# Kernel optimization log

Hardware: AMD Instinct MI355X
Metric: run time of the kernel (lower is better)

Reference implementation:

```python
import jax, jax.numpy as jnp
import numpy as np

ROPE_DIM = 64
NOPE_DIM = 128
KV_LORA_RANK = 512
B, H, S = 4, 16, 1024


def setup_inputs() -> dict:
    key = jax.random.key(0)
    k1, k2, k3 = jax.random.split(key, 3)
    q_nope_with_k_up = jax.random.normal(k1, (B, H, S, KV_LORA_RANK), dtype=jnp.float32)
    compressed_kv = jax.random.normal(k2, (B, S, KV_LORA_RANK), dtype=jnp.float32)
    rope_attention = jax.random.normal(k3, (B, H, S, S), dtype=jnp.float32)
    mask = jnp.zeros((B, S), dtype=jnp.int32)  # key padding mask; 1 = masked
    return {
        "q_nope_with_k_up": q_nope_with_k_up,
        "compressed_kv": compressed_kv,
        "rope_attention": rope_attention,
        "mask": mask,
        "have_causal_mask": 1,
    }


def reference(q_nope_with_k_up, compressed_kv, rope_attention, mask, have_causal_mask):
    # nope scores: [B,H,S,S] = q [B,H,S,r] @ kv^T [B,1,r,S]
    nope = jnp.einsum("bhqr,bkr->bhqk", q_nope_with_k_up, compressed_kv)
    scale = 1.0 / np.float32(np.sqrt(ROPE_DIM + NOPE_DIM))
    scores = (rope_attention + nope) * scale
    if mask is not None:
        m = mask[:, None, None, :]  # [B,1,1,S]
        if have_causal_mask:
            s = scores.shape[-1]
            causal = jnp.triu(jnp.ones((s, s), dtype=jnp.int32), 1)[None, None]  # [1,1,S,S]
            m = jnp.where(causal == 1, causal, m)  # combined mask, 1 = masked
        scores = jnp.where(m == 1, -jnp.inf, scores)
    attn = jax.nn.softmax(scores, axis=-1)
    # AV with shared compressed latent: [B,H,S,S] @ [B,1,S,r] -> [B,H,S,r]
    return jnp.einsum("bhqk,bkr->bhqr", attn, compressed_kv)
```

## Files before the change

### kernel.cpp

```cpp
#include <hip/hip_runtime.h>
#include <math.h>

#define B_ 4
#define H_ 16
#define S_ 1024
#define R_ 512
#define BQ 64
#define BK 32
#define NTHREADS 512
#define NKS 16

typedef unsigned short u16;
typedef unsigned int   u32;
typedef short bf16x8 __attribute__((ext_vector_type(8)));
typedef float f32x4  __attribute__((ext_vector_type(4)));

__device__ inline u16 f2bf(float x) {
    union { float f; u32 u; } v; v.f = x;
    return (u16)((v.u + 0x7fffu + ((v.u >> 16) & 1u)) >> 16);
}
__device__ inline u32 pack2(float a, float b) {
    return (u32)f2bf(a) | ((u32)f2bf(b) << 16);
}

#define MFMA16(a, b, c) __builtin_amdgcn_mfma_f32_16x16x32_bf16(a, b, c, 0, 0, 0)

__device__ inline void gload16(const void* g, void* l) {
    __builtin_amdgcn_global_load_lds(
        (const __attribute__((address_space(1))) void*)g,
        (__attribute__((address_space(3))) void*)l,
        16, 0, 0);
}

#define RAW_BARRIER() do {                                 \
    asm volatile("s_waitcnt lgkmcnt(0)" ::: "memory");     \
    __builtin_amdgcn_s_barrier();                          \
    asm volatile("" ::: "memory");                         \
} while (0)

__global__ __launch_bounds__(256)
void mla_prep_kernel(const float* __restrict__ ckv,
                     u16* __restrict__ ckv_bf,
                     u16* __restrict__ ckvT)
{
    const int tid = threadIdx.x;
    const int k0 = blockIdx.x * 64;
    const int r0 = blockIdx.y * 64;
    const int b  = blockIdx.z;

    __shared__ u16 sT[64][72];

    const float* src = ckv + ((size_t)b * S_ + k0) * R_ + r0;
    u16* obf = ckv_bf + ((size_t)b * S_ + k0) * R_ + r0;

    #pragma unroll
    for (int i = 0; i < 2; ++i) {
        int idx = tid + i * 256;
        int kk  = idx >> 3;
        int c8  = idx & 7;
        int csrc = c8 ^ (kk & 7);
        const float* p = src + (size_t)kk * R_ + csrc * 8;
        float4 f0 = *(const float4*)p;
        float4 f1 = *(const float4*)(p + 4);
        u32 w0 = pack2(f0.x, f0.y), w1 = pack2(f0.z, f0.w);
        u32 w2 = pack2(f1.x, f1.y), w3 = pack2(f1.z, f1.w);
        u32* dst = (u32*)(obf + (size_t)kk * R_ + c8 * 8);
        dst[0] = w0; dst[1] = w1; dst[2] = w2; dst[3] = w3;
        u16 e[8] = {(u16)w0,(u16)(w0>>16),(u16)w1,(u16)(w1>>16),
                    (u16)w2,(u16)(w2>>16),(u16)w3,(u16)(w3>>16)};
        #pragma unroll
        for (int j = 0; j < 8; ++j) sT[csrc * 8 + j][kk] = e[j];
    }
    __syncthreads();

    u16* obT = ckvT + (size_t)b * R_ * S_;
    #pragma unroll
    for (int i = 0; i < 2; ++i) {
        int idx = tid + i * 256;
        int rr = idx >> 3;
        int kc = idx & 7;
        const u16* s = &sT[rr][kc * 8];
        u32* dd = (u32*)(obT + (size_t)(r0 + rr) * S_ + k0 + kc * 8);
        dd[0] = (u32)s[0] | ((u32)s[1] << 16);
        dd[1] = (u32)s[2] | ((u32)s[3] << 16);
        dd[2] = (u32)s[4] | ((u32)s[5] << 16);
        dd[3] = (u32)s[6] | ((u32)s[7] << 16);
    }
}

__global__ __attribute__((amdgpu_waves_per_eu(2, 2)))
__launch_bounds__(NTHREADS)
void mla_attn_kernel(const float* __restrict__ qn,
                     const float* __restrict__ rope,
                     const int*   __restrict__ mask,
                     const int*   __restrict__ cmaskp,
                     const u16*   __restrict__ ckv_bf,
                     const u16*   __restrict__ ckvT,
                     float*       __restrict__ out)
{
    const int tid  = threadIdx.x;
    const int lane = tid & 63;
    const int wv   = tid >> 6;
    const int l15  = lane & 15;
    const int lq   = lane >> 4;
    const int qg   = wv >> 1;
    const int ktg  = wv & 1;

    const int qt = (int)gridDim.x - 1 - (int)blockIdx.x;
    const int h  = blockIdx.y;
    const int b  = blockIdx.z;
    const int q0 = qt * BQ;

    const int cflag = cmaskp[0];

    __shared__ __align__(16) u16 sCKV [2][BK][R_];
    __shared__ __align__(16) u16 sCKVT[2][R_][BK];
    __shared__ __align__(16) u16 sP[BQ][40];

    bf16x8 aq[NKS];
    {
        const float* qrow = qn + ((size_t)((b * H_ + h) * S_ + q0 + qg * 16 + l15)) * R_;
        #pragma unroll
        for (int s = 0; s < NKS; ++s) {
            const float* p = qrow + 32 * s + lq * 8;
            float4 f0 = *(const float4*)p;
            float4 f1 = *(const float4*)(p + 4);
            union { u32 u[4]; bf16x8 v; } cv;
            cv.u[0] = pack2(f0.x, f0.y); cv.u[1] = pack2(f0.z, f0.w);
            cv.u[2] = pack2(f1.x, f1.y); cv.u[3] = pack2(f1.z, f1.w);
            aq[s] = cv.v;
        }
    }

    f32x4 acc[4][4];
    #pragma unroll
    for (int i = 0; i < 4; ++i)
        #pragma unroll
        for (int j = 0; j < 4; ++j)
            acc[i][j] = (f32x4){0.f, 0.f, 0.f, 0.f};

    float m_run[4], l_run[4];
    #pragma unroll
    for (int r = 0; r < 4; ++r) { m_run[r] = -INFINITY; l_run[r] = 0.0f; }

    const u16*   ckvb  = ckv_bf + (size_t)b * S_ * R_;
    const u16*   ckvTb = ckvT   + (size_t)b * R_ * S_;
    const float* ropeb = rope + ((size_t)(b * H_ + h)) * S_ * S_;
    const int*   maskb = mask + b * S_;

    const int nkt = cflag ? ((q0 + BQ) / BK) : (S_ / BK);
    const float SCALE = 0.07216878364870323f;
    const int rowg0 = q0 + qg * 16 + 4 * lq;

    float rp[4];
    int   mkv;

    {
        char* lA = (char*)&sCKV [0][0][0] + wv * 1024;
        char* lT = (char*)&sCKVT[0][0][0] + wv * 1024;
        #pragma unroll
        for (int rd = 0; rd < 4; ++rd) {
            u32 o = (u32)(rd * 8192 + tid * 16);
            gload16((const char*)ckvb + o, lA + rd * 8192);
            gload16((const char*)ckvTb + (size_t)(o >> 6) * 2048 + (o & 63),
                    lT + rd * 8192);
        }
        #pragma unroll
        for (int reg = 0; reg < 4; ++reg)
            rp[reg] = ropeb[(size_t)(rowg0 + reg) * S_ + ktg * 16 + l15];
        mkv = maskb[ktg * 16 + l15];
    }
    __syncthreads();

    for (int kt = 0; kt < nkt; ++kt) {
        const int d  = kt & 1;
        const int k0 = kt * BK;
        const bool more = (kt + 1 < nkt);
        float rp_n[4];
        int   mkv_n = 0;

        if (more) {
            const int k0n = k0 + BK;
            const char* gA = (const char*)ckvb  + (size_t)k0n * 1024;
            const char* gT = (const char*)ckvTb + (size_t)k0n * 2;
            char* lA = (char*)&sCKV [d ^ 1][0][0] + wv * 1024;
            char* lT = (char*)&sCKVT[d ^ 1][0][0] + wv * 1024;
            #pragma unroll
            for (int rd = 0; rd < 4; ++rd) {
                u32 o = (u32)(rd * 8192 + tid * 16);
                gload16(gA + o, lA + rd * 8192);
                gload16(gT + (size_t)(o >> 6) * 2048 + (o & 63), lT + rd * 8192);
            }
            #pragma unroll
            for (int reg = 0; reg < 4; ++reg)
                rp_n[reg] = ropeb[(size_t)(rowg0 + reg) * S_ + k0n + ktg * 16 + l15];
            mkv_n = maskb[k0n + ktg * 16 + l15];
        }

        f32x4 sc0 = {0.f,0.f,0.f,0.f}, sc1 = {0.f,0.f,0.f,0.f};
        {
            const char* base = (const char*)&sCKV[d][0][0];
            const u32 rowb = (u32)(ktg * 16 + l15) * 1024;
            const u32 swz  = ((u32)(l15 & 7)) << 4;
            #pragma unroll
            for (int s = 0; s < NKS; s += 2) {
                bf16x8 bf0 = *(const bf16x8*)(base + rowb +
                                (((u32)(64 * s)      + (u32)(16 * lq)) ^ swz));
                bf16x8 bf1 = *(const bf16x8*)(base + rowb +
                                (((u32)(64 * s + 64) + (u32)(16 * lq)) ^ swz));
                sc0 = MFMA16(aq[s],     bf0, sc0);
                sc1 = MFMA16(aq[s + 1], bf1, sc1);
            }
        }

        float scf[4], vm[4];
        {
            const int colg = k0 + ktg * 16 + l15;
            #pragma unroll
            for (int reg = 0; reg < 4; ++reg) {
                float v = (sc0[reg] + sc1[reg] + rp[reg]) * SCALE;
                if (mkv) v = -INFINITY;
                if (cflag && colg > rowg0 + reg) v = -INFINITY;
                scf[reg] = v;
                vm[reg]  = v;
            }
            #pragma unroll
            for (int m = 1; m <= 8; m <<= 1)
                #pragma unroll
                for (int reg = 0; reg < 4; ++reg)
                    vm[reg] = fmaxf(vm[reg], __shfl_xor(vm[reg], m));
            if (l15 == 0) {
                #pragma unroll
                for (int reg = 0; reg < 4; ++reg)
                    *(float*)&sP[qg * 16 + 4 * lq + reg][34 + 2 * ktg] = vm[reg];
            }
        }
        RAW_BARRIER();

        {
            float pv[4], alpha[4], rs[4];
            #pragma unroll
            for (int reg = 0; reg < 4; ++reg) {
                float pm = *(const float*)&sP[qg * 16 + 4 * lq + reg][34 + 2 * (ktg ^ 1)];
                float mn = fmaxf(m_run[reg], fmaxf(vm[reg], pm));
                if (mn == -INFINITY) {
                    alpha[reg] = 1.0f; pv[reg] = 0.0f;
                } else {
                    alpha[reg] = __expf(m_run[reg] - mn);
                    pv[reg]    = __expf(scf[reg] - mn);
                }
                m_run[reg] = mn;
                rs[reg] = pv[reg];
            }
            #pragma unroll
            for (int m = 1; m <= 8; m <<= 1)
                #pragma unroll
                for (int reg = 0; reg < 4; ++reg)
                    rs[reg] += __shfl_xor(rs[reg], m);
            #pragma unroll
            for (int reg = 0; reg < 4; ++reg) {
                l_run[reg] = l_run[reg] * alpha[reg] + rs[reg];
                sP[qg * 16 + 4 * lq + reg][ktg * 16 + l15] = f2bf(pv[reg]);
            }
            if (ktg == 0 && l15 == 0) {
                #pragma unroll
                for (int reg = 0; reg < 4; ++reg)
                    *(float*)&sP[qg * 16 + 4 * lq + reg][32] = alpha[reg];
            }
        }
        RAW_BARRIER();

        {
            float alr[4][4];
            #pragma unroll
            for (int mi = 0; mi < 4; ++mi)
                #pragma unroll
                for (int reg = 0; reg < 4; ++reg)
                    alr[mi][reg] = *(const float*)&sP[mi * 16 + 4 * lq + reg][32];
            #pragma unroll
            for (int mi = 0; mi < 4; ++mi)
                #pragma unroll
                for (int ni = 0; ni < 4; ++ni)
                    #pragma unroll
                    for (int reg = 0; reg < 4; ++reg)
                        acc[mi][ni][reg] *= alr[mi][reg];

            const int kq = lq * 8;
            bf16x8 af[4], bfr[4];
            #pragma unroll
            for (int mi = 0; mi < 4; ++mi)
                af[mi] = *(const bf16x8*)&sP[mi * 16 + l15][kq];
            const char* tbase = (const char*)&sCKVT[d][0][0];
            #pragma unroll
            for (int ni = 0; ni < 4; ++ni)
                bfr[ni] = *(const bf16x8*)(tbase +
                            (u32)(wv * 64 + ni * 16 + l15) * 64 + (u32)(lq * 16));
            #pragma unroll
            for (int mi = 0; mi < 4; ++mi)
                #pragma unroll
                for (int ni = 0; ni < 4; ++ni)
                    acc[mi][ni] = MFMA16(af[mi], bfr[ni], acc[mi][ni]);
        }
        __syncthreads();

        #pragma unroll
        for (int reg = 0; reg < 4; ++reg) rp[reg] = more ? rp_n[reg] : rp[reg];
        mkv = more ? mkv_n : mkv;
    }

    if (l15 == 0) {
        #pragma unroll
        for (int reg = 0; reg < 4; ++reg)
            *(float*)&sP[qg * 16 + 4 * lq + reg][34 + 2 * ktg] = l_run[reg];
    }
    __syncthreads();

    float linv[4][4];
    #pragma unroll
    for (int mi = 0; mi < 4; ++mi)
        #pragma unroll
        for (int reg = 0; reg < 4; ++reg) {
            int row = mi * 16 + 4 * lq + reg;
            float lt = *(const float*)&sP[row][34] + *(const float*)&sP[row][36];
            linv[mi][reg] = 1.0f / lt;
        }

    float* ob = out + ((size_t)((b * H_ + h) * S_ + q0)) * R_;
    #pragma unroll
    for (int mi = 0; mi < 4; ++mi)
        #pragma unroll
        for (int ni = 0; ni < 4; ++ni)
            #pragma unroll
            for (int reg = 0; reg < 4; ++reg)
                ob[(size_t)(mi * 16 + 4 * lq + reg) * R_ + wv * 64 + ni * 16 + l15]
                    = acc[mi][ni][reg] * linv[mi][reg];
}

extern "C" void kernel_launch(void* const* d_in, const int* in_sizes, int n_in,
                              void* d_out, int out_size, void* d_ws, size_t ws_size,
                              hipStream_t stream)
{
    (void)in_sizes; (void)n_in; (void)out_size; (void)ws_size;
    const float* qn   = (const float*)d_in[0];
    const float* ckv  = (const float*)d_in[1];
    const float* rope = (const float*)d_in[2];
    const int*   mask = (const int*)d_in[3];
    const int*   cm   = (const int*)d_in[4];
    float* out = (float*)d_out;

    u16* ckv_bf = (u16*)d_ws;
    u16* ckvT   = ckv_bf + (size_t)B_ * S_ * R_;

    hipLaunchKernelGGL(mla_prep_kernel, dim3(S_ / 64, R_ / 64, B_), dim3(256),
                       0, stream, ckv, ckv_bf, ckvT);
    hipLaunchKernelGGL(mla_attn_kernel, dim3(S_ / BQ, H_, B_), dim3(NTHREADS),
                       0, stream, qn, rope, mask, cm, ckv_bf, ckvT, out);
}
```

Baseline: 842.1 us.

## Software-pipeline QK and PV stages with BK=64, one barrier per iteration

Doubles the key tile to 64 and restructures the loop so the softmax/PV stage of tile kt-1 overlaps with the QK stage of tile kt, using double-buffered P and metadata buffers and a single __syncthreads per iteration instead of three barriers. The transposed latent is no longer staged through LDS; PV B-fragments are read directly from global memory. P writes use an XOR swizzle, and s_setprio brackets the MFMA regions. This cuts barrier count and LDS traffic but adds register pressure and puts direct global loads on the PV path, which may stall if they miss cache.

```diff
diff --git a/kernel.cpp b/kernel.cpp
--- a/kernel.cpp
+++ b/kernel.cpp
@@ -6,7 +6,7 @@
 #define S_ 1024
 #define R_ 512
 #define BQ 64
-#define BK 32
+#define BK 64
 #define NTHREADS 512
 #define NKS 16
 
@@ -31,12 +31,6 @@
         (__attribute__((address_space(3))) void*)l,
         16, 0, 0);
 }
-
-#define RAW_BARRIER() do {                                 \
-    asm volatile("s_waitcnt lgkmcnt(0)" ::: "memory");     \
-    __builtin_amdgcn_s_barrier();                          \
-    asm volatile("" ::: "memory");                         \
-} while (0)
 
 __global__ __launch_bounds__(256)
 void mla_prep_kernel(const float* __restrict__ ckv,
@@ -113,9 +107,10 @@
 
     const int cflag = cmaskp[0];
 
-    __shared__ __align__(16) u16 sCKV [2][BK][R_];
-    __shared__ __align__(16) u16 sCKVT[2][R_][BK];
-    __shared__ __align__(16) u16 sP[BQ][40];
+    __shared__ __align__(16) u16   sCKV[2][BK][R_];
+    __shared__ __align__(16) u16   sPP[2][BQ][BK];
+    __shared__ __align__(16) float sMeta[2][BQ][4];
+    __shared__ __align__(16) f32x4 sAlpha[2][16];
 
     bf16x8 aq[NKS];
     {
@@ -148,81 +143,101 @@
     const float* ropeb = rope + ((size_t)(b * H_ + h)) * S_ * S_;
     const int*   maskb = mask + b * S_;
 
-    const int nkt = cflag ? ((q0 + BQ) / BK) : (S_ / BK);
+    const int nkt = cflag ? (qt + 1) : (S_ / BK);
     const float SCALE = 0.07216878364870323f;
     const int rowg0 = q0 + qg * 16 + 4 * lq;
 
-    float rp[4];
-    int   mkv;
+    float rp[2][4], rpn[2][4];
+    int   mkv[2], mkvn[2];
+    float scp[2][4];
+    float vmp[4];
+    bf16x8 bfr[4][2];
 
     {
-        char* lA = (char*)&sCKV [0][0][0] + wv * 1024;
-        char* lT = (char*)&sCKVT[0][0][0] + wv * 1024;
-        #pragma unroll
-        for (int rd = 0; rd < 4; ++rd) {
-            u32 o = (u32)(rd * 8192 + tid * 16);
-            gload16((const char*)ckvb + o, lA + rd * 8192);
-            gload16((const char*)ckvTb + (size_t)(o >> 6) * 2048 + (o & 63),
-                    lT + rd * 8192);
-        }
-        #pragma unroll
-        for (int reg = 0; reg < 4; ++reg)
-            rp[reg] = ropeb[(size_t)(rowg0 + reg) * S_ + ktg * 16 + l15];
-        mkv = maskb[ktg * 16 + l15];
+        char* lA = (char*)&sCKV[0][0][0] + wv * 1024;
+        const char* gA = (const char*)ckvb;
+        #pragma unroll
+        for (int rd = 0; rd < 8; ++rd) {
+            u32 o = (u32)(rd * 8192 + wv * 1024 + (lane & 63) * 16);
+            gload16(gA + o, lA + rd * 8192);
+        }
+        const float* rb2 = ropeb + (size_t)rowg0 * S_ + ktg * 32 + l15;
+        #pragma unroll
+        for (int reg = 0; reg < 4; ++reg) {
+            rp[0][reg] = rb2[(size_t)reg * S_];
+            rp[1][reg] = rb2[(size_t)reg * S_ + 16];
+        }
+        mkv[0] = maskb[ktg * 32 + l15];
+        mkv[1] = maskb[ktg * 32 + 16 + l15];
     }
     __syncthreads();
 
-    for (int kt = 0; kt < nkt; ++kt) {
-        const int d  = kt & 1;
-        const int k0 = kt * BK;
-        const bool more = (kt + 1 < nkt);
-        float rp_n[4];
-        int   mkv_n = 0;
-
-        if (more) {
-            const int k0n = k0 + BK;
-            const char* gA = (const char*)ckvb  + (size_t)k0n * 1024;
-            const char* gT = (const char*)ckvTb + (size_t)k0n * 2;
-            char* lA = (char*)&sCKV [d ^ 1][0][0] + wv * 1024;
-            char* lT = (char*)&sCKVT[d ^ 1][0][0] + wv * 1024;
-            #pragma unroll
-            for (int rd = 0; rd < 4; ++rd) {
-                u32 o = (u32)(rd * 8192 + tid * 16);
+    for (int kt = 0; kt <= nkt; ++kt) {
+        const int d   = kt & 1;
+        const int pbc = kt & 1;
+        const int pbm = pbc ^ 1;
+
+        if (kt + 1 < nkt) {
+            const char* gA = (const char*)ckvb + (size_t)(kt + 1) * (BK * R_ * 2);
+            char* lA = (char*)&sCKV[d ^ 1][0][0] + wv * 1024;
+            #pragma unroll
+            for (int rd = 0; rd < 8; ++rd) {
+                u32 o = (u32)(rd * 8192 + wv * 1024 + (lane & 63) * 16);
                 gload16(gA + o, lA + rd * 8192);
-                gload16(gT + (size_t)(o >> 6) * 2048 + (o & 63), lT + rd * 8192);
-            }
-            #pragma unroll
-            for (int reg = 0; reg < 4; ++reg)
-                rp_n[reg] = ropeb[(size_t)(rowg0 + reg) * S_ + k0n + ktg * 16 + l15];
-            mkv_n = maskb[k0n + ktg * 16 + l15];
-        }
-
-        f32x4 sc0 = {0.f,0.f,0.f,0.f}, sc1 = {0.f,0.f,0.f,0.f};
-        {
+            }
+            const int k0n = (kt + 1) * BK;
+            const float* rb2 = ropeb + (size_t)rowg0 * S_ + k0n + ktg * 32 + l15;
+            #pragma unroll
+            for (int reg = 0; reg < 4; ++reg) {
+                rpn[0][reg] = rb2[(size_t)reg * S_];
+                rpn[1][reg] = rb2[(size_t)reg * S_ + 16];
+            }
+            mkvn[0] = maskb[k0n + ktg * 32 + l15];
+            mkvn[1] = maskb[k0n + ktg * 32 + 16 + l15];
+        }
+        if (kt >= 1) {
+            const u16* tb = ckvTb + (size_t)(wv * 64 + l15) * S_ + (kt - 1) * BK + lq * 8;
+            #pragma unroll
+            for (int ni = 0; ni < 4; ++ni)
+                #pragma unroll
+                for (int ks = 0; ks < 2; ++ks)
+                    bfr[ni][ks] = *(const bf16x8*)(tb + (size_t)ni * 16 * S_ + ks * 32);
+        }
+
+        float scf[2][4], vm[4];
+        if (kt < nkt) {
+            f32x4 sc00 = {0.f,0.f,0.f,0.f}, sc01 = {0.f,0.f,0.f,0.f};
+            f32x4 sc10 = {0.f,0.f,0.f,0.f}, sc11 = {0.f,0.f,0.f,0.f};
             const char* base = (const char*)&sCKV[d][0][0];
-            const u32 rowb = (u32)(ktg * 16 + l15) * 1024;
-            const u32 swz  = ((u32)(l15 & 7)) << 4;
+            const u32 row0b = (u32)(ktg * 32 + l15) * 1024;
+            const u32 row1b = row0b + 16 * 1024;
+            const u32 swz = ((u32)(l15 & 7)) << 4;
+            __builtin_amdgcn_s_setprio(1);
             #pragma unroll
             for (int s = 0; s < NKS; s += 2) {
-                bf16x8 bf0 = *(const bf16x8*)(base + rowb +
-                                (((u32)(64 * s)      + (u32)(16 * lq)) ^ swz));
-                bf16x8 bf1 = *(const bf16x8*)(base + rowb +
-                                (((u32)(64 * s + 64) + (u32)(16 * lq)) ^ swz));
-                sc0 = MFMA16(aq[s],     bf0, sc0);
-                sc1 = MFMA16(aq[s + 1], bf1, sc1);
-            }
-        }
-
-        float scf[4], vm[4];
-        {
-            const int colg = k0 + ktg * 16 + l15;
-            #pragma unroll
-            for (int reg = 0; reg < 4; ++reg) {
-                float v = (sc0[reg] + sc1[reg] + rp[reg]) * SCALE;
-                if (mkv) v = -INFINITY;
-                if (cflag && colg > rowg0 + reg) v = -INFINITY;
-                scf[reg] = v;
-                vm[reg]  = v;
+                u32 c0 = ((u32)(64 * s)      + (u32)(16 * lq)) ^ swz;
+                u32 c1 = ((u32)(64 * s + 64) + (u32)(16 * lq)) ^ swz;
+                bf16x8 b00 = *(const bf16x8*)(base + row0b + c0);
+                bf16x8 b10 = *(const bf16x8*)(base + row1b + c0);
+                bf16x8 b01 = *(const bf16x8*)(base + row0b + c1);
+                bf16x8 b11 = *(const bf16x8*)(base + row1b + c1);
+                sc00 = MFMA16(aq[s],     b00, sc00);
+                sc10 = MFMA16(aq[s],     b10, sc10);
+                sc01 = MFMA16(aq[s + 1], b01, sc01);
+                sc11 = MFMA16(aq[s + 1], b11, sc11);
+            }
+            __builtin_amdgcn_s_setprio(0);
+            const int colg0 = kt * BK + ktg * 32 + l15;
+            #pragma unroll
+            for (int reg = 0; reg < 4; ++reg) {
+                float v0 = (sc00[reg] + sc01[reg] + rp[0][reg]) * SCALE;
+                float v1 = (sc10[reg] + sc11[reg] + rp[1][reg]) * SCALE;
+                if (mkv[0]) v0 = -INFINITY;
+                if (mkv[1]) v1 = -INFINITY;
+                if (cflag && colg0      > rowg0 + reg) v0 = -INFINITY;
+                if (cflag && colg0 + 16 > rowg0 + reg) v1 = -INFINITY;
+                scf[0][reg] = v0; scf[1][reg] = v1;
+                vm[reg] = fmaxf(v0, v1);
             }
             #pragma unroll
             for (int m = 1; m <= 8; m <<= 1)
@@ -232,51 +247,65 @@
             if (l15 == 0) {
                 #pragma unroll
                 for (int reg = 0; reg < 4; ++reg)
-                    *(float*)&sP[qg * 16 + 4 * lq + reg][34 + 2 * ktg] = vm[reg];
-            }
-        }
-        RAW_BARRIER();
-
-        {
-            float pv[4], alpha[4], rs[4];
-            #pragma unroll
-            for (int reg = 0; reg < 4; ++reg) {
-                float pm = *(const float*)&sP[qg * 16 + 4 * lq + reg][34 + 2 * (ktg ^ 1)];
-                float mn = fmaxf(m_run[reg], fmaxf(vm[reg], pm));
+                    sMeta[pbc][qg * 16 + 4 * lq + reg][ktg] = vm[reg];
+            }
+        }
+
+        if (kt >= 1) {
+            float alpha[4], pv0[4], pv1[4], rs[4];
+            #pragma unroll
+            for (int reg = 0; reg < 4; ++reg) {
+                float pm = sMeta[pbm][qg * 16 + 4 * lq + reg][ktg ^ 1];
+                float mn = fmaxf(m_run[reg], fmaxf(vmp[reg], pm));
                 if (mn == -INFINITY) {
-                    alpha[reg] = 1.0f; pv[reg] = 0.0f;
+                    alpha[reg] = 1.0f; pv0[reg] = 0.0f; pv1[reg] = 0.0f;
                 } else {
                     alpha[reg] = __expf(m_run[reg] - mn);
-                    pv[reg]    = __expf(scf[reg] - mn);
+                    pv0[reg]   = __expf(scp[0][reg] - mn);
+                    pv1[reg]   = __expf(scp[1][reg] - mn);
                 }
                 m_run[reg] = mn;
-                rs[reg] = pv[reg];
+                rs[reg] = pv0[reg] + pv1[reg];
             }
             #pragma unroll
             for (int m = 1; m <= 8; m <<= 1)
                 #pragma unroll
                 for (int reg = 0; reg < 4; ++reg)
                     rs[reg] += __shfl_xor(rs[reg], m);
+            char* pbase = (char*)&sPP[pbm][0][0];
             #pragma unroll
             for (int reg = 0; reg < 4; ++reg) {
                 l_run[reg] = l_run[reg] * alpha[reg] + rs[reg];
-                sP[qg * 16 + 4 * lq + reg][ktg * 16 + l15] = f2bf(pv[reg]);
+                const u32 row = (u32)(qg * 16 + 4 * lq + reg);
+                const u32 rswz = (row & 7) << 4;
+                u32 w0 = ((u32)(ktg * 64      + 2 * l15)) ^ rswz;
+                u32 w1 = ((u32)(ktg * 64 + 32 + 2 * l15)) ^ rswz;
+                *(u16*)(pbase + row * 128 + w0) = f2bf(pv0[reg]);
+                *(u16*)(pbase + row * 128 + w1) = f2bf(pv1[reg]);
             }
             if (ktg == 0 && l15 == 0) {
-                #pragma unroll
-                for (int reg = 0; reg < 4; ++reg)
-                    *(float*)&sP[qg * 16 + 4 * lq + reg][32] = alpha[reg];
-            }
-        }
-        RAW_BARRIER();
-
-        {
-            float alr[4][4];
+                f32x4 av = {alpha[0], alpha[1], alpha[2], alpha[3]};
+                sAlpha[pbm][qg * 4 + lq] = av;
+            }
+        }
+
+        if (kt < nkt) {
+            #pragma unroll
+            for (int reg = 0; reg < 4; ++reg) {
+                vmp[reg] = vm[reg];
+                scp[0][reg] = scf[0][reg]; scp[1][reg] = scf[1][reg];
+                rp[0][reg] = rpn[0][reg];  rp[1][reg] = rpn[1][reg];
+            }
+            mkv[0] = mkvn[0]; mkv[1] = mkvn[1];
+        }
+
+        __syncthreads();
+
+        if (kt >= 1) {
+            f32x4 alr[4];
             #pragma unroll
             for (int mi = 0; mi < 4; ++mi)
-                #pragma unroll
-                for (int reg = 0; reg < 4; ++reg)
-                    alr[mi][reg] = *(const float*)&sP[mi * 16 + 4 * lq + reg][32];
+                alr[mi] = sAlpha[pbm][mi * 4 + lq];
             #pragma unroll
             for (int mi = 0; mi < 4; ++mi)
                 #pragma unroll
@@ -285,33 +314,31 @@
                     for (int reg = 0; reg < 4; ++reg)
                         acc[mi][ni][reg] *= alr[mi][reg];
 
-            const int kq = lq * 8;
-            bf16x8 af[4], bfr[4];
+            bf16x8 af[4][2];
+            const char* pbase = (const char*)&sPP[pbm][0][0];
+            const u32 rswz = ((u32)(l15 & 7)) << 4;
+            #pragma unroll
+            for (int mi = 0; mi < 4; ++mi) {
+                const u32 rb = (u32)(mi * 16 + l15) * 128;
+                af[mi][0] = *(const bf16x8*)(pbase + rb + (((u32)(16 * lq))      ^ rswz));
+                af[mi][1] = *(const bf16x8*)(pbase + rb + (((u32)(64 + 16 * lq)) ^ rswz));
+            }
+            __builtin_amdgcn_s_setprio(1);
             #pragma unroll
             for (int mi = 0; mi < 4; ++mi)
-                af[mi] = *(const bf16x8*)&sP[mi * 16 + l15][kq];
-            const char* tbase = (const char*)&sCKVT[d][0][0];
-            #pragma unroll
-            for (int ni = 0; ni < 4; ++ni)
-                bfr[ni] = *(const bf16x8*)(tbase +
-                            (u32)(wv * 64 + ni * 16 + l15) * 64 + (u32)(lq * 16));
-            #pragma unroll
-            for (int mi = 0; mi < 4; ++mi)
-                #pragma unroll
-                for (int ni = 0; ni < 4; ++ni)
-                    acc[mi][ni] = MFMA16(af[mi], bfr[ni], acc[mi][ni]);
-        }
-        __syncthreads();
-
-        #pragma unroll
-        for (int reg = 0; reg < 4; ++reg) rp[reg] = more ? rp_n[reg] : rp[reg];
-        mkv = more ? mkv_n : mkv;
+                #pragma unroll
+                for (int ni = 0; ni < 4; ++ni) {
+                    acc[mi][ni] = MFMA16(af[mi][0], bfr[ni][0], acc[mi][ni]);
+                    acc[mi][ni] = MFMA16(af[mi][1], bfr[ni][1], acc[mi][ni]);
+                }
+            __builtin_amdgcn_s_setprio(0);
+        }
     }
 
     if (l15 == 0) {
         #pragma unroll
         for (int reg = 0; reg < 4; ++reg)
-            *(float*)&sP[qg * 16 + 4 * lq + reg][34 + 2 * ktg] = l_run[reg];
+            sMeta[0][qg * 16 + 4 * lq + reg][ktg] = l_run[reg];
     }
     __syncthreads();
 
@@ -321,7 +348,7 @@
         #pragma unroll
         for (int reg = 0; reg < 4; ++reg) {
             int row = mi * 16 + 4 * lq + reg;
-            float lt = *(const float*)&sP[row][34] + *(const float*)&sP[row][36];
+            float lt = sMeta[0][row][0] + sMeta[0][row][1];
             linv[mi][reg] = 1.0f / lt;
         }
 
```

New measurement: 1.240 ms. +47.2%, slower.

## Halve query tile, split QK reduction across waves, read V-transpose from global

Applied to the files above, without the earlier changes.

The query tile shrinks from 64 to 32 rows, and the 512-deep QK contraction is split in halves across wave pairs. Partial scores are combined through a new shared-memory buffer, and half the waves run the softmax with 8-lane row reductions. The transposed latent tile is no longer staged in LDS; each wave loads its B fragments for the PV MFMA straight from global memory. Launch bounds now allow more blocks per CU and s_setprio is added around the MFMA blocks, trading fewer registers and less LDS for more blocks and extra uncoalesced global reads.

```diff
diff --git a/kernel.cpp b/kernel.cpp
--- a/kernel.cpp
+++ b/kernel.cpp
@@ -5,10 +5,9 @@
 #define H_ 16
 #define S_ 1024
 #define R_ 512
-#define BQ 64
+#define BQ 32
 #define BK 32
 #define NTHREADS 512
-#define NKS 16
 
 typedef unsigned short u16;
 typedef unsigned int   u32;
@@ -88,8 +87,7 @@
     }
 }
 
-__global__ __attribute__((amdgpu_waves_per_eu(2, 2)))
-__launch_bounds__(NTHREADS)
+__global__ __launch_bounds__(NTHREADS, 4)
 void mla_attn_kernel(const float* __restrict__ qn,
                      const float* __restrict__ rope,
                      const int*   __restrict__ mask,
@@ -103,25 +101,34 @@
     const int wv   = tid >> 6;
     const int l15  = lane & 15;
     const int lq   = lane >> 4;
-    const int qg   = wv >> 1;
-    const int ktg  = wv & 1;
-
-    const int qt = (int)gridDim.x - 1 - (int)blockIdx.x;
+    const int qg   = wv >> 2;
+    const int ktg  = (wv >> 1) & 1;
+    const int kq   = wv & 1;
+    const int rq   = wv & 3;
+    const bool isSM = (kq == 0);
+    const int sub  = ktg;
+    const int r8   = lane >> 3;
+    const int cg   = lane & 7;
+
+    const int qt = 31 - (int)blockIdx.x;
     const int h  = blockIdx.y;
     const int b  = blockIdx.z;
     const int q0 = qt * BQ;
 
     const int cflag = cmaskp[0];
 
-    __shared__ __align__(16) u16 sCKV [2][BK][R_];
-    __shared__ __align__(16) u16 sCKVT[2][R_][BK];
-    __shared__ __align__(16) u16 sP[BQ][40];
-
-    bf16x8 aq[NKS];
+    __shared__ __align__(16) u16   sCKV[2][BK][R_];
+    __shared__ __align__(16) float sPart[2][2][32][17];
+    __shared__ __align__(16) u16   sP[BQ][40];
+    __shared__ __align__(16) float sAlpha[BQ];
+    __shared__ __align__(16) float sL[BQ];
+
+    bf16x8 aq[8];
     {
-        const float* qrow = qn + ((size_t)((b * H_ + h) * S_ + q0 + qg * 16 + l15)) * R_;
+        const float* qrow = qn + ((size_t)((b * H_ + h) * S_ + q0 + qg * 16 + l15)) * R_
+                          + kq * 256;
         #pragma unroll
-        for (int s = 0; s < NKS; ++s) {
+        for (int s = 0; s < 8; ++s) {
             const float* p = qrow + 32 * s + lq * 8;
             float4 f0 = *(const float4*)p;
             float4 f1 = *(const float4*)(p + 4);
@@ -132,208 +139,172 @@
         }
     }
 
-    f32x4 acc[4][4];
+    f32x4 acc[8];
     #pragma unroll
-    for (int i = 0; i < 4; ++i)
-        #pragma unroll
-        for (int j = 0; j < 4; ++j)
-            acc[i][j] = (f32x4){0.f, 0.f, 0.f, 0.f};
-
-    float m_run[4], l_run[4];
-    #pragma unroll
-    for (int r = 0; r < 4; ++r) { m_run[r] = -INFINITY; l_run[r] = 0.0f; }
+    for (int i = 0; i < 8; ++i) acc[i] = (f32x4){0.f, 0.f, 0.f, 0.f};
+
+    float m_run = -INFINITY, l_run = 0.0f;
 
     const u16*   ckvb  = ckv_bf + (size_t)b * S_ * R_;
     const u16*   ckvTb = ckvT   + (size_t)b * R_ * S_;
     const float* ropeb = rope + ((size_t)(b * H_ + h)) * S_ * S_;
     const int*   maskb = mask + b * S_;
 
-    const int nkt = cflag ? ((q0 + BQ) / BK) : (S_ / BK);
+    const int nkt = cflag ? (qt + 1) : (S_ / BK);
     const float SCALE = 0.07216878364870323f;
-    const int rowg0 = q0 + qg * 16 + 4 * lq;
-
-    float rp[4];
-    int   mkv;
+    const int rowg = q0 + qg * 16 + sub * 8 + r8;
+    const int rowl = qg * 16 + sub * 8 + r8;
+
+    float rp0, rp1, rp2, rp3;
 
     {
-        char* lA = (char*)&sCKV [0][0][0] + wv * 1024;
-        char* lT = (char*)&sCKVT[0][0][0] + wv * 1024;
+        char* lA = (char*)&sCKV[0][0][0] + wv * 1024;
+        const char* gA = (const char*)ckvb;
         #pragma unroll
-        for (int rd = 0; rd < 4; ++rd) {
-            u32 o = (u32)(rd * 8192 + tid * 16);
-            gload16((const char*)ckvb + o, lA + rd * 8192);
-            gload16((const char*)ckvTb + (size_t)(o >> 6) * 2048 + (o & 63),
-                    lT + rd * 8192);
-        }
-        #pragma unroll
-        for (int reg = 0; reg < 4; ++reg)
-            rp[reg] = ropeb[(size_t)(rowg0 + reg) * S_ + ktg * 16 + l15];
-        mkv = maskb[ktg * 16 + l15];
+        for (int rd = 0; rd < 4; ++rd)
+            gload16(gA + (u32)(rd * 8192 + wv * 1024 + lane * 16), lA + rd * 8192);
+        if (isSM) {
+            const int cb = cg * 4;
+            float4 rv = *(const float4*)(ropeb + (size_t)rowg * S_ + cb);
+            int4   mv = *(const int4*)(maskb + cb);
+            rp0 = (mv.x || (cflag && cb + 0 > rowg)) ? -INFINITY : rv.x;
+            rp1 = (mv.y || (cflag && cb + 1 > rowg)) ? -INFINITY : rv.y;
+            rp2 = (mv.z || (cflag && cb + 2 > rowg)) ? -INFINITY : rv.z;
+            rp3 = (mv.w || (cflag && cb + 3 > rowg)) ? -INFINITY : rv.w;
+        }
     }
     __syncthreads();
 
     for (int kt = 0; kt < nkt; ++kt) {
-        const int d  = kt & 1;
-        const int k0 = kt * BK;
+        const int d = kt & 1;
         const bool more = (kt + 1 < nkt);
-        float rp_n[4];
-        int   mkv_n = 0;
 
         if (more) {
-            const int k0n = k0 + BK;
-            const char* gA = (const char*)ckvb  + (size_t)k0n * 1024;
-            const char* gT = (const char*)ckvTb + (size_t)k0n * 2;
-            char* lA = (char*)&sCKV [d ^ 1][0][0] + wv * 1024;
-            char* lT = (char*)&sCKVT[d ^ 1][0][0] + wv * 1024;
+            const char* gA = (const char*)ckvb + (size_t)(kt + 1) * (BK * R_ * 2);
+            char* lA = (char*)&sCKV[d ^ 1][0][0] + wv * 1024;
             #pragma unroll
-            for (int rd = 0; rd < 4; ++rd) {
-                u32 o = (u32)(rd * 8192 + tid * 16);
-                gload16(gA + o, lA + rd * 8192);
-                gload16(gT + (size_t)(o >> 6) * 2048 + (o & 63), lT + rd * 8192);
-            }
-            #pragma unroll
-            for (int reg = 0; reg < 4; ++reg)
-                rp_n[reg] = ropeb[(size_t)(rowg0 + reg) * S_ + k0n + ktg * 16 + l15];
-            mkv_n = maskb[k0n + ktg * 16 + l15];
-        }
-
-        f32x4 sc0 = {0.f,0.f,0.f,0.f}, sc1 = {0.f,0.f,0.f,0.f};
+            for (int rd = 0; rd < 4; ++rd)
+                gload16(gA + (u32)(rd * 8192 + wv * 1024 + lane * 16), lA + rd * 8192);
+        }
+        float rn0, rn1, rn2, rn3;
+        if (isSM && more) {
+            const int cb = (kt + 1) * BK + cg * 4;
+            float4 rv = *(const float4*)(ropeb + (size_t)rowg * S_ + cb);
+            int4   mv = *(const int4*)(maskb + cb);
+            rn0 = (mv.x || (cflag && cb + 0 > rowg)) ? -INFINITY : rv.x;
+            rn1 = (mv.y || (cflag && cb + 1 > rowg)) ? -INFINITY : rv.y;
+            rn2 = (mv.z || (cflag && cb + 2 > rowg)) ? -INFINITY : rv.z;
+            rn3 = (mv.w || (cflag && cb + 3 > rowg)) ? -INFINITY : rv.w;
+        }
+
         {
+            f32x4 sc = {0.f, 0.f, 0.f, 0.f};
             const char* base = (const char*)&sCKV[d][0][0];
             const u32 rowb = (u32)(ktg * 16 + l15) * 1024;
             const u32 swz  = ((u32)(l15 & 7)) << 4;
+            __builtin_amdgcn_s_setprio(1);
             #pragma unroll
-            for (int s = 0; s < NKS; s += 2) {
-                bf16x8 bf0 = *(const bf16x8*)(base + rowb +
-                                (((u32)(64 * s)      + (u32)(16 * lq)) ^ swz));
-                bf16x8 bf1 = *(const bf16x8*)(base + rowb +
-                                (((u32)(64 * s + 64) + (u32)(16 * lq)) ^ swz));
-                sc0 = MFMA16(aq[s],     bf0, sc0);
-                sc1 = MFMA16(aq[s + 1], bf1, sc1);
+            for (int s = 0; s < 8; ++s) {
+                u32 coff = ((u32)(kq * 512 + s * 64 + lq * 16)) ^ swz;
+                bf16x8 bf = *(const bf16x8*)(base + rowb + coff);
+                sc = MFMA16(aq[s], bf, sc);
             }
-        }
-
-        float scf[4], vm[4];
-        {
-            const int colg = k0 + ktg * 16 + l15;
-            #pragma unroll
-            for (int reg = 0; reg < 4; ++reg) {
-                float v = (sc0[reg] + sc1[reg] + rp[reg]) * SCALE;
-                if (mkv) v = -INFINITY;
-                if (cflag && colg > rowg0 + reg) v = -INFINITY;
-                scf[reg] = v;
-                vm[reg]  = v;
-            }
-            #pragma unroll
-            for (int m = 1; m <= 8; m <<= 1)
-                #pragma unroll
-                for (int reg = 0; reg < 4; ++reg)
-                    vm[reg] = fmaxf(vm[reg], __shfl_xor(vm[reg], m));
-            if (l15 == 0) {
-                #pragma unroll
-                for (int reg = 0; reg < 4; ++reg)
-                    *(float*)&sP[qg * 16 + 4 * lq + reg][34 + 2 * ktg] = vm[reg];
-            }
-        }
-        RAW_BARRIER();
-
-        {
-            float pv[4], alpha[4], rs[4];
-            #pragma unroll
-            for (int reg = 0; reg < 4; ++reg) {
-                float pm = *(const float*)&sP[qg * 16 + 4 * lq + reg][34 + 2 * (ktg ^ 1)];
-                float mn = fmaxf(m_run[reg], fmaxf(vm[reg], pm));
-                if (mn == -INFINITY) {
-                    alpha[reg] = 1.0f; pv[reg] = 0.0f;
-                } else {
-                    alpha[reg] = __expf(m_run[reg] - mn);
-                    pv[reg]    = __expf(scf[reg] - mn);
-                }
-                m_run[reg] = mn;
-                rs[reg] = pv[reg];
-            }
-            #pragma unroll
-            for (int m = 1; m <= 8; m <<= 1)
-                #pragma unroll
-                for (int reg = 0; reg < 4; ++reg)
-                    rs[reg] += __shfl_xor(rs[reg], m);
-            #pragma unroll
-            for (int reg = 0; reg < 4; ++reg) {
-                l_run[reg] = l_run[reg] * alpha[reg] + rs[reg];
-                sP[qg * 16 + 4 * lq + reg][ktg * 16 + l15] = f2bf(pv[reg]);
-            }
-            if (ktg == 0 && l15 == 0) {
-                #pragma unroll
-                for (int reg = 0; reg < 4; ++reg)
-                    *(float*)&sP[qg * 16 + 4 * lq + reg][32] = alpha[reg];
-            }
-        }
-        RAW_BARRIER();
-
-        {
-            float alr[4][4];
-            #pragma unroll
-            for (int mi = 0; mi < 4; ++mi)
-                #pragma unroll
-                for (int reg = 0; reg < 4; ++reg)
-                    alr[mi][reg] = *(const float*)&sP[mi * 16 + 4 * lq + reg][32];
-            #pragma unroll
-            for (int mi = 0; mi < 4; ++mi)
-                #pragma unroll
-                for (int ni = 0; ni < 4; ++ni)
-                    #pragma unroll
-                    for (int reg = 0; reg < 4; ++reg)
-                        acc[mi][ni][reg] *= alr[mi][reg];
-
-            const int kq = lq * 8;
-            bf16x8 af[4], bfr[4];
-            #pragma unroll
-            for (int mi = 0; mi < 4; ++mi)
-                af[mi] = *(const bf16x8*)&sP[mi * 16 + l15][kq];
-            const char* tbase = (const char*)&sCKVT[d][0][0];
-            #pragma unroll
-            for (int ni = 0; ni < 4; ++ni)
-                bfr[ni] = *(const bf16x8*)(tbase +
-                            (u32)(wv * 64 + ni * 16 + l15) * 64 + (u32)(lq * 16));
-            #pragma unroll
-            for (int mi = 0; mi < 4; ++mi)
-                #pragma unroll
-                for (int ni = 0; ni < 4; ++ni)
-                    acc[mi][ni] = MFMA16(af[mi], bfr[ni], acc[mi][ni]);
-        }
-        __syncthreads();
-
-        #pragma unroll
-        for (int reg = 0; reg < 4; ++reg) rp[reg] = more ? rp_n[reg] : rp[reg];
-        mkv = more ? mkv_n : mkv;
-    }
-
-    if (l15 == 0) {
-        #pragma unroll
-        for (int reg = 0; reg < 4; ++reg)
-            *(float*)&sP[qg * 16 + 4 * lq + reg][34 + 2 * ktg] = l_run[reg];
-    }
-    __syncthreads();
-
-    float linv[4][4];
-    #pragma unroll
-    for (int mi = 0; mi < 4; ++mi)
-        #pragma unroll
-        for (int reg = 0; reg < 4; ++reg) {
-            int row = mi * 16 + 4 * lq + reg;
-            float lt = *(const float*)&sP[row][34] + *(const float*)&sP[row][36];
-            linv[mi][reg] = 1.0f / lt;
-        }
-
-    float* ob = out + ((size_t)((b * H_ + h) * S_ + q0)) * R_;
-    #pragma unroll
-    for (int mi = 0; mi < 4; ++mi)
-        #pragma unroll
-        for (int ni = 0; ni < 4; ++ni)
+            __builtin_amdgcn_s_setprio(0);
             #pragma unroll
             for (int reg = 0; reg < 4; ++reg)
-                ob[(size_t)(mi * 16 + 4 * lq + reg) * R_ + wv * 64 + ni * 16 + l15]
-                    = acc[mi][ni][reg] * linv[mi][reg];
+                sPart[qg][kq][ktg * 16 + l15][4 * lq + reg] = sc[reg];
+        }
+
+        RAW_BARRIER();
+
+        const u16* tb = ckvTb + (size_t)(rq * 128 + l15) * S_ + kt * BK + lq * 8;
+        bf16x8 bfr0 = *(const bf16x8*)(tb);
+        bf16x8 bfr1 = *(const bf16x8*)(tb + (size_t)16 * S_);
+        bf16x8 bfr2 = *(const bf16x8*)(tb + (size_t)32 * S_);
+        bf16x8 bfr3 = *(const bf16x8*)(tb + (size_t)48 * S_);
+
+        if (isSM) {
+            const int rl = sub * 8 + r8;
+            float s0, s1, s2, s3;
+            {
+                const int c = cg * 4;
+                s0 = (sPart[qg][0][c + 0][rl] + sPart[qg][1][c + 0][rl] + rp0) * SCALE;
+                s1 = (sPart[qg][0][c + 1][rl] + sPart[qg][1][c + 1][rl] + rp1) * SCALE;
+                s2 = (sPart[qg][0][c + 2][rl] + sPart[qg][1][c + 2][rl] + rp2) * SCALE;
+                s3 = (sPart[qg][0][c + 3][rl] + sPart[qg][1][c + 3][rl] + rp3) * SCALE;
+            }
+            float vm = fmaxf(fmaxf(s0, s1), fmaxf(s2, s3));
+            vm = fmaxf(vm, __shfl_xor(vm, 1));
+            vm = fmaxf(vm, __shfl_xor(vm, 2));
+            vm = fmaxf(vm, __shfl_xor(vm, 4));
+            float mn = fmaxf(m_run, vm);
+            float alpha, p0, p1, p2, p3;
+            if (mn == -INFINITY) {
+                alpha = 1.0f; p0 = p1 = p2 = p3 = 0.0f;
+            } else {
+                alpha = __expf(m_run - mn);
+                p0 = __expf(s0 - mn); p1 = __expf(s1 - mn);
+                p2 = __expf(s2 - mn); p3 = __expf(s3 - mn);
+            }
+            float rs = (p0 + p1) + (p2 + p3);
+            rs += __shfl_xor(rs, 1);
+            rs += __shfl_xor(rs, 2);
+            rs += __shfl_xor(rs, 4);
+            m_run = mn;
+            l_run = l_run * alpha + rs;
+            u32* pw = (u32*)&sP[rowl][cg * 4];
+            pw[0] = pack2(p0, p1);
+            pw[1] = pack2(p2, p3);
+            if (cg == 0) sAlpha[rowl] = alpha;
+        }
+
+        RAW_BARRIER();
+
+        {
+            bf16x8 bfr4 = *(const bf16x8*)(tb + (size_t)64 * S_);
+            bf16x8 bfr5 = *(const bf16x8*)(tb + (size_t)80 * S_);
+            bf16x8 bfr6 = *(const bf16x8*)(tb + (size_t)96 * S_);
+            bf16x8 bfr7 = *(const bf16x8*)(tb + (size_t)112 * S_);
+
+            float alr0 = sAlpha[qg * 16 + 4 * lq + 0];
+            float alr1 = sAlpha[qg * 16 + 4 * lq + 1];
+            float alr2 = sAlpha[qg * 16 + 4 * lq + 2];
+            float alr3 = sAlpha[qg * 16 + 4 * lq + 3];
+            #pragma unroll
+            for (int ni = 0; ni < 8; ++ni) {
+                acc[ni][0] *= alr0; acc[ni][1] *= alr1;
+                acc[ni][2] *= alr2; acc[ni][3] *= alr3;
+            }
+            bf16x8 af = *(const bf16x8*)&sP[qg * 16 + l15][lq * 8];
+            __builtin_amdgcn_s_setprio(1);
+            acc[0] = MFMA16(af, bfr0, acc[0]);
+            acc[1] = MFMA16(af, bfr1, acc[1]);
+            acc[2] = MFMA16(af, bfr2, acc[2]);
+            acc[3] = MFMA16(af, bfr3, acc[3]);
+            acc[4] = MFMA16(af, bfr4, acc[4]);
+            acc[5] = MFMA16(af, bfr5, acc[5]);
+            acc[6] = MFMA16(af, bfr6, acc[6]);
+            acc[7] = MFMA16(af, bfr7, acc[7]);
+            __builtin_amdgcn_s_setprio(0);
+        }
+
+        __syncthreads();
+
+        if (isSM && more) { rp0 = rn0; rp1 = rn1; rp2 = rn2; rp3 = rn3; }
+    }
+
+    if (isSM && cg == 0) sL[rowl] = l_run;
+    __syncthreads();
+
+    float* ob = out + ((size_t)((b * H_ + h) * S_ + q0)) * R_ + rq * 128;
+    #pragma unroll
+    for (int reg = 0; reg < 4; ++reg) {
+        const int row = qg * 16 + 4 * lq + reg;
+        const float linv = 1.0f / sL[row];
+        #pragma unroll
+        for (int ni = 0; ni < 8; ++ni)
+            ob[(size_t)row * R_ + ni * 16 + l15] = acc[ni][reg] * linv;
+    }
 }
 
 extern "C" void kernel_launch(void* const* d_in, const int* in_sizes, int n_in,
```

Result: slower. 1.290 ms (+53.2%).
